# Performance work log

Hardware: AMD Instinct MI355X
Metric: run time of the kernel (lower is better)

## Reference

```python
import jax, jax.numpy as jnp
import numpy as np

INPUT_SIZE = 16
HIDDEN = 256


def setup_inputs() -> dict:
    key = jax.random.key(0)
    ks = jax.random.split(key, 12)
    B, T, F, H = 512, 168, INPUT_SIZE, HIDDEN
    s_ih = 1.0 / np.sqrt(H)
    def u(k, shape):
        return jax.random.uniform(k, shape, jnp.float32, -s_ih, s_ih)
    return {
        "x": jax.random.normal(ks[0], (B, T, F), jnp.float32),
        # LSTM params, torch gate order (i, f, g, o) stacked along dim 0
        "w_ih": u(ks[1], (4 * H, F)),
        "w_hh": u(ks[2], (4 * H, H)),
        "b_ih": u(ks[3], (4 * H,)),
        "b_hh": u(ks[4], (4 * H,)),
        # MLP params
        "fc1_w": u(ks[5], (128, H)),
        "fc1_b": u(ks[6], (128,)),
        "fc2_w": u(ks[7], (64, 128)),
        "fc2_b": u(ks[8], (64,)),
        "fc3_w": u(ks[9], (1, 64)),
        "fc3_b": u(ks[10], (1,)),
    }


def _lstm(x, w_ih, w_hh, b_ih, b_hh):
    B, T, F = x.shape
    H = w_hh.shape[1]
    # Precompute input contribution for all timesteps: [B, T, 4H]
    x_proj = jnp.einsum("btf,gf->btg", x, w_ih) + b_ih + b_hh

    def step(carry, xp_t):
        h, c = carry
        gates = xp_t + h @ w_hh.T  # [B, 4H]
        i, f, g, o = jnp.split(gates, 4, axis=-1)
        i = jax.nn.sigmoid(i)
        f = jax.nn.sigmoid(f)
        g = jnp.tanh(g)
        o = jax.nn.sigmoid(o)
        c = f * c + i * g
        h = o * jnp.tanh(c)
        return (h, c), h

    h0 = jnp.zeros((B, H), x.dtype)
    c0 = jnp.zeros((B, H), x.dtype)
    (_, _), hs = jax.lax.scan(step, (h0, c0), jnp.swapaxes(x_proj, 0, 1))
    return jnp.swapaxes(hs, 0, 1)  # [B, T, H]


def reference(x, w_ih, w_hh, b_ih, b_hh, fc1_w, fc1_b, fc2_w, fc2_b, fc3_w, fc3_b):
    h = _lstm(x, w_ih, w_hh, b_ih, b_hh)          # [B, T, H]
    h = jax.nn.relu(h @ fc1_w.T + fc1_b)           # [B, T, 128]
    h = jax.nn.relu(h @ fc2_w.T + fc2_b)           # [B, T, 64]
    out = h @ fc3_w.T + fc3_b                      # [B, T, 1]
    return out
```

## Files before the change

### kernel.cpp

```cpp
#include <hip/hip_runtime.h>

typedef _Float16 half8 __attribute__((ext_vector_type(8)));
typedef float floatx4 __attribute__((ext_vector_type(4)));
typedef unsigned uint4v __attribute__((ext_vector_type(4)));

#define Bsz 512
#define Tsz 168
#define Fsz 16
#define Hsz 256
#define KTILES 9
#define LDS_K 296

#define WSW_OFF   0
#define BIAS_OFF  589824
#define HH_OFF    675840
#define XBUF_OFF  (HH_OFF + 44040192)

__global__ __launch_bounds__(256) void k_prep(
    const float* __restrict__ w_hh, const float* __restrict__ w_ih,
    const float* __restrict__ b_ih, const float* __restrict__ b_hh,
    _Float16* __restrict__ wsw, float* __restrict__ bias) {
    const int b = blockIdx.x, tid = threadIdx.x;
    const int lane = tid & 63, sub = tid >> 6;
    if (b < 144) {
        int tile = b * 4 + sub;
        int nt = tile / KTILES, kt = tile - nt * KTILES;
        int n_in = lane & 15, kg = lane >> 4;
        int J = nt >> 2, g = nt & 3;
        int n_orig = g * 256 + J * 16 + n_in;
        half8 v;
#pragma unroll
        for (int e = 0; e < 8; ++e) {
            int k = kt * 32 + kg * 8 + e;
            float f;
            if (k < 256)      f = w_hh[n_orig * 256 + k];
            else if (k < 272) f = w_ih[n_orig * 16 + (k - 256)];
            else              f = 0.0f;
            v[e] = (_Float16)f;
        }
        ((half8*)wsw)[tile * 64 + lane] = v;
    } else {
        int id = (b - 144) * 256 + tid;
        int nt = id >> 4, n = id & 15;
        int J = nt >> 2, g = nt & 3;
        int n_orig = g * 256 + J * 16 + n;
        bias[id] = b_ih[n_orig] + b_hh[n_orig];
    }
}

__global__ __launch_bounds__(512, 2) void k_lstm16(
    const float* __restrict__ x, const _Float16* __restrict__ wsw,
    const float* __restrict__ bias, unsigned* __restrict__ hh32,
    unsigned long long* __restrict__ xbuf) {
    __shared__ __align__(16) _Float16 h_lds[16][LDS_K];
    __shared__ float glds[4][16][68];

    const int tid = threadIdx.x;
    const int wave = tid >> 6, lane = tid & 63;
    const int n_in = lane & 15, quad = lane >> 4;
    const int bb = blockIdx.x & 31, ng = blockIdx.x >> 5;
    const int b0 = bb * 16;
    const int Jl = wave & 3;
    const int gp = wave >> 2;

    float bs[2];
    uint4v wf[2][KTILES];
#pragma unroll
    for (int gg = 0; gg < 2; ++gg) {
        const int nt = ng * 16 + Jl * 4 + gp * 2 + gg;
        bs[gg] = bias[nt * 16 + n_in];
#pragma unroll
        for (int kt = 0; kt < KTILES; ++kt)
            wf[gg][kt] = ((const uint4v*)wsw)[((size_t)nt * KTILES + kt) * 64 + lane];
    }
#pragma unroll
    for (int gg = 0; gg < 2; ++gg) {
        asm volatile("" : "+v"(bs[gg]));
#pragma unroll
        for (int kt = 0; kt < KTILES; ++kt)
            asm volatile("" : "+v"(wf[gg][kt]));
    }

    for (int i = tid; i < 16 * LDS_K; i += 512)
        ((_Float16*)h_lds)[i] = (_Float16)0.0f;
    __syncthreads();
    if (tid < 256) {
        int m = tid >> 4, f = tid & 15;
        h_lds[m][Hsz + f] = (_Float16)x[((b0 + m) * Tsz + 0) * Fsz + f];
    }
    __syncthreads();

    const int cm = tid >> 5, cj = tid & 31;
    float c_st[2] = {0.f, 0.f};

    for (int t = 0; t < Tsz; ++t) {
        float xr = 0.0f;
        if (t + 1 < Tsz && tid < 256)
            xr = x[((b0 + (tid >> 4)) * Tsz + (t + 1)) * Fsz + (tid & 15)];

        half8 afr[KTILES];
#pragma unroll
        for (int kt = 0; kt < KTILES; ++kt)
            afr[kt] = *(const half8*)&h_lds[n_in][kt * 32 + quad * 8];

        floatx4 acc[2] = {(floatx4){0.f,0.f,0.f,0.f}, (floatx4){0.f,0.f,0.f,0.f}};
#pragma unroll
        for (int gg = 0; gg < 2; ++gg) {
#pragma unroll
            for (int kt = 0; kt < KTILES; ++kt)
                acc[gg] = __builtin_amdgcn_mfma_f32_16x16x32_f16(
                    afr[kt], __builtin_bit_cast(half8, wf[gg][kt]), acc[gg], 0, 0, 0);
        }

#pragma unroll
        for (int gg = 0; gg < 2; ++gg)
#pragma unroll
            for (int r = 0; r < 4; ++r)
                glds[gp * 2 + gg][quad * 4 + r][Jl * 16 + n_in] = acc[gg][r] + bs[gg];
        __syncthreads();

        union { _Float16 f[2]; unsigned u; } pk;
#pragma unroll
        for (int e = 0; e < 2; ++e) {
            int jl = 2 * cj + e;
            float ig = glds[0][cm][jl];
            float fg = glds[1][cm][jl];
            float gg_ = glds[2][cm][jl];
            float og = glds[3][cm][jl];
            float si = 1.0f / (1.0f + __expf(-ig));
            float sf = 1.0f / (1.0f + __expf(-fg));
            float tg = 1.0f - 2.0f / (__expf(2.0f * gg_) + 1.0f);
            float so = 1.0f / (1.0f + __expf(-og));
            float c = sf * c_st[e] + si * tg;
            c_st[e] = c;
            float th = 1.0f - 2.0f / (__expf(2.0f * c) + 1.0f);
            pk.f[e] = (_Float16)(so * th);
        }

        const size_t rb = ((size_t)((bb * 2 + (t & 1)) * 16));
        if (t + 1 < Tsz) {
            unsigned long long pv = ((unsigned long long)pk.u << 32) | (unsigned)(t + 1);
            __hip_atomic_store(&xbuf[(rb + cm) * 128 + ng * 32 + cj], pv,
                               __ATOMIC_RELAXED, __HIP_MEMORY_SCOPE_AGENT);
        }
        *(unsigned*)&h_lds[cm][ng * 64 + 2 * cj] = pk.u;
        __builtin_nontemporal_store(
            pk.u, &hh32[((size_t)(b0 + cm) * Tsz + t) * 128 + ng * 32 + cj]);

        if (t + 1 < Tsz) {
            const unsigned want = (unsigned)(t + 1);
            unsigned long long* p1 = &xbuf[(rb + cm) * 128 + ((ng + 1) & 3) * 32 + cj];
            unsigned long long* p2 = &xbuf[(rb + cm) * 128 + ((ng + 2) & 3) * 32 + cj];
            unsigned long long* p3 = &xbuf[(rb + cm) * 128 + ((ng + 3) & 3) * 32 + cj];
            unsigned long long v1 = __hip_atomic_load(p1, __ATOMIC_RELAXED,
                                                      __HIP_MEMORY_SCOPE_AGENT);
            unsigned long long v2 = __hip_atomic_load(p2, __ATOMIC_RELAXED,
                                                      __HIP_MEMORY_SCOPE_AGENT);
            unsigned long long v3 = __hip_atomic_load(p3, __ATOMIC_RELAXED,
                                                      __HIP_MEMORY_SCOPE_AGENT);
            while ((unsigned)v1 != want || (unsigned)v2 != want || (unsigned)v3 != want) {
                v1 = __hip_atomic_load(p1, __ATOMIC_RELAXED, __HIP_MEMORY_SCOPE_AGENT);
                v2 = __hip_atomic_load(p2, __ATOMIC_RELAXED, __HIP_MEMORY_SCOPE_AGENT);
                v3 = __hip_atomic_load(p3, __ATOMIC_RELAXED, __HIP_MEMORY_SCOPE_AGENT);
            }
            *(unsigned*)&h_lds[cm][((ng + 1) & 3) * 64 + 2 * cj] = (unsigned)(v1 >> 32);
            *(unsigned*)&h_lds[cm][((ng + 2) & 3) * 64 + 2 * cj] = (unsigned)(v2 >> 32);
            *(unsigned*)&h_lds[cm][((ng + 3) & 3) * 64 + 2 * cj] = (unsigned)(v3 >> 32);
            if (tid < 256)
                h_lds[tid >> 4][Hsz + (tid & 15)] = (_Float16)xr;
            __syncthreads();
        }
    }
}

__global__ __launch_bounds__(512, 2) void k_mlp6(
    const _Float16* __restrict__ hh, const float* __restrict__ fc1_w,
    const float* __restrict__ fc2_w, const float* __restrict__ b1,
    const float* __restrict__ b2, const float* __restrict__ w3,
    const float* __restrict__ b3, float* __restrict__ out) {
    __shared__ __align__(16) _Float16 w1sh[64 * 512];
    __shared__ __align__(16) _Float16 w2sh[16 * 512];
    __shared__ _Float16 st1[8][16][136];
    __shared__ _Float16 st2[8][16][72];

    const int tid = threadIdx.x;
    const int wave = tid >> 6, lane = tid & 63;
    const int n_in = lane & 15, quad = lane >> 4;

    {
#pragma unroll
        for (int it = 0; it < 8; ++it) {
            int s = it * 512 + tid;
            int tile = s >> 6, ln = s & 63;
            int nt = tile >> 3, kt = tile & 7, ni = ln & 15, kg = ln >> 4;
            const float* src = &fc1_w[(nt * 16 + ni) * 256 + kt * 32 + kg * 8];
            half8 v;
#pragma unroll
            for (int e = 0; e < 8; ++e) v[e] = (_Float16)src[e];
            ((half8*)w1sh)[s] = v;
        }
#pragma unroll
        for (int it = 0; it < 2; ++it) {
            int s = it * 512 + tid;
            int tile = s >> 6, ln = s & 63;
            int nt = tile >> 2, kt = tile & 3, ni = ln & 15, kg = ln >> 4;
            const float* src = &fc2_w[(nt * 16 + ni) * 128 + kt * 32 + kg * 8];
            half8 v;
#pragma unroll
            for (int e = 0; e < 8; ++e) v[e] = (_Float16)src[e];
            ((half8*)w2sh)[s] = v;
        }
    }
    __syncthreads();

    uint4v bufA[8], bufB[8], bufC[8];
    const int ch0 = blockIdx.x, ch1 = blockIdx.x + 224, ch2 = blockIdx.x + 448;

#define MLP_LOAD(dst, ch)                                                      \
    {                                                                          \
        const int tok0_ = (ch) * 128 + wave * 16;                              \
        _Pragma("unroll")                                                      \
        for (int kt = 0; kt < 8; ++kt)                                         \
            dst[kt] = __builtin_nontemporal_load(                              \
                (const uint4v*)&hh[(size_t)(tok0_ + n_in) * 256 + kt * 32 +    \
                                   quad * 8]);                                 \
    }

    MLP_LOAD(bufA, ch0)
    MLP_LOAD(bufB, ch1)
    MLP_LOAD(bufC, ch2)

    auto compute = [&](const uint4v* raw, int chunk) {
        const int tok0 = chunk * 128 + wave * 16;
        half8 afr[8];
#pragma unroll
        for (int kt = 0; kt < 8; ++kt)
            afr[kt] = __builtin_bit_cast(half8, raw[kt]);

#pragma unroll
        for (int nt = 0; nt < 8; ++nt) {
            floatx4 a = (floatx4){0.f, 0.f, 0.f, 0.f};
#pragma unroll
            for (int kt = 0; kt < 8; ++kt) {
                half8 bfr = *(const half8*)&w1sh[(nt * 8 + kt) * 512 + lane * 8];
                a = __builtin_amdgcn_mfma_f32_16x16x32_f16(afr[kt], bfr, a, 0, 0, 0);
            }
            float bbv = b1[nt * 16 + n_in];
#pragma unroll
            for (int r = 0; r < 4; ++r) {
                float v = a[r] + bbv;
                st1[wave][quad * 4 + r][nt * 16 + n_in] = (_Float16)(v > 0.f ? v : 0.f);
            }
        }

        half8 a2[4];
#pragma unroll
        for (int kt = 0; kt < 4; ++kt)
            a2[kt] = *(const half8*)&st1[wave][n_in][kt * 32 + quad * 8];
#pragma unroll
        for (int nt = 0; nt < 4; ++nt) {
            floatx4 a = (floatx4){0.f, 0.f, 0.f, 0.f};
#pragma unroll
            for (int kt = 0; kt < 4; ++kt) {
                half8 bfr = *(const half8*)&w2sh[(nt * 4 + kt) * 512 + lane * 8];
                a = __builtin_amdgcn_mfma_f32_16x16x32_f16(a2[kt], bfr, a, 0, 0, 0);
            }
            float bbv = b2[nt * 16 + n_in];
#pragma unroll
            for (int r = 0; r < 4; ++r) {
                float v = a[r] + bbv;
                st2[wave][quad * 4 + r][nt * 16 + n_in] = (_Float16)(v > 0.f ? v : 0.f);
            }
        }

        float p = 0.0f;
#pragma unroll
        for (int e = 0; e < 16; ++e)
            p += (float)st2[wave][n_in][quad * 16 + e] * w3[quad * 16 + e];
        p += __shfl_down(p, 32);
        p += __shfl_down(p, 16);
        if (quad == 0) out[tok0 + n_in] = p + b3[0];
    };

    compute(bufA, ch0);
    compute(bufB, ch1);
    compute(bufC, ch2);
#undef MLP_LOAD
}

extern "C" void kernel_launch(void* const* d_in, const int* in_sizes, int n_in,
                              void* d_out, int out_size, void* d_ws, size_t ws_size,
                              hipStream_t stream) {
    const float* x     = (const float*)d_in[0];
    const float* w_ih  = (const float*)d_in[1];
    const float* w_hh  = (const float*)d_in[2];
    const float* b_ih  = (const float*)d_in[3];
    const float* b_hh  = (const float*)d_in[4];
    const float* fc1_w = (const float*)d_in[5];
    const float* fc1_b = (const float*)d_in[6];
    const float* fc2_w = (const float*)d_in[7];
    const float* fc2_b = (const float*)d_in[8];
    const float* fc3_w = (const float*)d_in[9];
    const float* fc3_b = (const float*)d_in[10];

    char* ws = (char*)d_ws;
    _Float16* wsw  = (_Float16*)(ws + WSW_OFF);
    float*    bias = (float*)(ws + BIAS_OFF);
    _Float16* hhist= (_Float16*)(ws + HH_OFF);
    unsigned long long* xbuf = (unsigned long long*)(ws + XBUF_OFF);

    k_prep<<<148, 256, 0, stream>>>(w_hh, w_ih, b_ih, b_hh, wsw, bias);
    k_lstm16<<<128, 512, 0, stream>>>(x, wsw, bias, (unsigned*)hhist, xbuf);
    k_mlp6<<<224, 512, 0, stream>>>(hhist, fc1_w, fc2_w, fc1_b, fc2_b,
                                    fc3_w, fc3_b, (float*)d_out);
}
```

Before: 489.1 us.

## Split LSTM hidden dimension across eight blocks per batch tile instead of four

The recurrent LSTM kernel now launches 256 blocks, so eight blocks share a 16-row batch tile and each owns 32 hidden units, halving per-wave MFMA work and register-resident weights. Each block now polls seven peer slots per step instead of three in the global exchange buffer, and the xbuf row stride doubles. This aims to shorten each sequential step's compute on the critical path by using more CUs, at the cost of more cross-block synchronisation traffic and polling latency. The x prefetch was also moved after the h store.

```diff
diff --git a/kernel.cpp b/kernel.cpp
--- a/kernel.cpp
+++ b/kernel.cpp
@@ -48,38 +48,27 @@
     }
 }
 
-__global__ __launch_bounds__(512, 2) void k_lstm16(
+__global__ __launch_bounds__(512, 1) void k_lstm17(
     const float* __restrict__ x, const _Float16* __restrict__ wsw,
     const float* __restrict__ bias, unsigned* __restrict__ hh32,
     unsigned long long* __restrict__ xbuf) {
     __shared__ __align__(16) _Float16 h_lds[16][LDS_K];
-    __shared__ float glds[4][16][68];
+    __shared__ float glds[4][16][36];
 
     const int tid = threadIdx.x;
     const int wave = tid >> 6, lane = tid & 63;
     const int n_in = lane & 15, quad = lane >> 4;
     const int bb = blockIdx.x & 31, ng = blockIdx.x >> 5;
     const int b0 = bb * 16;
-    const int Jl = wave & 3;
-    const int gp = wave >> 2;
-
-    float bs[2];
-    uint4v wf[2][KTILES];
-#pragma unroll
-    for (int gg = 0; gg < 2; ++gg) {
-        const int nt = ng * 16 + Jl * 4 + gp * 2 + gg;
-        bs[gg] = bias[nt * 16 + n_in];
-#pragma unroll
-        for (int kt = 0; kt < KTILES; ++kt)
-            wf[gg][kt] = ((const uint4v*)wsw)[((size_t)nt * KTILES + kt) * 64 + lane];
-    }
-#pragma unroll
-    for (int gg = 0; gg < 2; ++gg) {
-        asm volatile("" : "+v"(bs[gg]));
-#pragma unroll
-        for (int kt = 0; kt < KTILES; ++kt)
-            asm volatile("" : "+v"(wf[gg][kt]));
-    }
+    const int Jl = wave & 1;
+    const int g  = wave >> 1;
+    const int nt = (ng * 2 + Jl) * 4 + g;
+
+    const float bs = bias[nt * 16 + n_in];
+    half8 wf[KTILES];
+#pragma unroll
+    for (int kt = 0; kt < KTILES; ++kt)
+        wf[kt] = ((const half8*)wsw)[((size_t)nt * KTILES + kt) * 64 + lane];
 
     for (int i = tid; i < 16 * LDS_K; i += 512)
         ((_Float16*)h_lds)[i] = (_Float16)0.0f;
@@ -91,81 +80,81 @@
     __syncthreads();
 
     const int cm = tid >> 5, cj = tid & 31;
-    float c_st[2] = {0.f, 0.f};
+    float c_st = 0.f;
+    unsigned short* hh16 = (unsigned short*)hh32;
 
     for (int t = 0; t < Tsz; ++t) {
-        float xr = 0.0f;
-        if (t + 1 < Tsz && tid < 256)
-            xr = x[((b0 + (tid >> 4)) * Tsz + (t + 1)) * Fsz + (tid & 15)];
-
         half8 afr[KTILES];
 #pragma unroll
         for (int kt = 0; kt < KTILES; ++kt)
             afr[kt] = *(const half8*)&h_lds[n_in][kt * 32 + quad * 8];
 
-        floatx4 acc[2] = {(floatx4){0.f,0.f,0.f,0.f}, (floatx4){0.f,0.f,0.f,0.f}};
-#pragma unroll
-        for (int gg = 0; gg < 2; ++gg) {
-#pragma unroll
-            for (int kt = 0; kt < KTILES; ++kt)
-                acc[gg] = __builtin_amdgcn_mfma_f32_16x16x32_f16(
-                    afr[kt], __builtin_bit_cast(half8, wf[gg][kt]), acc[gg], 0, 0, 0);
-        }
-
-#pragma unroll
-        for (int gg = 0; gg < 2; ++gg)
-#pragma unroll
-            for (int r = 0; r < 4; ++r)
-                glds[gp * 2 + gg][quad * 4 + r][Jl * 16 + n_in] = acc[gg][r] + bs[gg];
+        floatx4 acc = (floatx4){0.f, 0.f, 0.f, 0.f};
+#pragma unroll
+        for (int kt = 0; kt < KTILES; ++kt)
+            acc = __builtin_amdgcn_mfma_f32_16x16x32_f16(afr[kt], wf[kt], acc, 0, 0, 0);
+
+#pragma unroll
+        for (int r = 0; r < 4; ++r)
+            glds[g][quad * 4 + r][Jl * 16 + n_in] = acc[r] + bs;
         __syncthreads();
 
-        union { _Float16 f[2]; unsigned u; } pk;
-#pragma unroll
-        for (int e = 0; e < 2; ++e) {
-            int jl = 2 * cj + e;
-            float ig = glds[0][cm][jl];
-            float fg = glds[1][cm][jl];
-            float gg_ = glds[2][cm][jl];
-            float og = glds[3][cm][jl];
-            float si = 1.0f / (1.0f + __expf(-ig));
-            float sf = 1.0f / (1.0f + __expf(-fg));
-            float tg = 1.0f - 2.0f / (__expf(2.0f * gg_) + 1.0f);
-            float so = 1.0f / (1.0f + __expf(-og));
-            float c = sf * c_st[e] + si * tg;
-            c_st[e] = c;
-            float th = 1.0f - 2.0f / (__expf(2.0f * c) + 1.0f);
-            pk.f[e] = (_Float16)(so * th);
-        }
+        float ig = glds[0][cm][cj];
+        float fg = glds[1][cm][cj];
+        float gv = glds[2][cm][cj];
+        float og = glds[3][cm][cj];
+        float si = 1.0f / (1.0f + __expf(-ig));
+        float sf = 1.0f / (1.0f + __expf(-fg));
+        float tg = 1.0f - 2.0f / (__expf(2.0f * gv) + 1.0f);
+        float so = 1.0f / (1.0f + __expf(-og));
+        float c = sf * c_st + si * tg;
+        c_st = c;
+        float th = 1.0f - 2.0f / (__expf(2.0f * c) + 1.0f);
+        _Float16 hval = (_Float16)(so * th);
+        unsigned short hu = __builtin_bit_cast(unsigned short, hval);
+
+        h_lds[cm][ng * 32 + cj] = hval;
 
         const size_t rb = ((size_t)((bb * 2 + (t & 1)) * 16));
         if (t + 1 < Tsz) {
-            unsigned long long pv = ((unsigned long long)pk.u << 32) | (unsigned)(t + 1);
-            __hip_atomic_store(&xbuf[(rb + cm) * 128 + ng * 32 + cj], pv,
+            unsigned long long pv =
+                ((unsigned long long)hu << 32) | (unsigned)(t + 1);
+            __hip_atomic_store(&xbuf[(rb + cm) * 256 + ng * 32 + cj], pv,
                                __ATOMIC_RELAXED, __HIP_MEMORY_SCOPE_AGENT);
         }
-        *(unsigned*)&h_lds[cm][ng * 64 + 2 * cj] = pk.u;
         __builtin_nontemporal_store(
-            pk.u, &hh32[((size_t)(b0 + cm) * Tsz + t) * 128 + ng * 32 + cj]);
+            hu, &hh16[((size_t)(b0 + cm) * Tsz + t) * 256 + ng * 32 + cj]);
 
         if (t + 1 < Tsz) {
+            float xr = 0.0f;
+            if (tid < 256)
+                xr = x[((b0 + (tid >> 4)) * Tsz + (t + 1)) * Fsz + (tid & 15)];
+
             const unsigned want = (unsigned)(t + 1);
-            unsigned long long* p1 = &xbuf[(rb + cm) * 128 + ((ng + 1) & 3) * 32 + cj];
-            unsigned long long* p2 = &xbuf[(rb + cm) * 128 + ((ng + 2) & 3) * 32 + cj];
-            unsigned long long* p3 = &xbuf[(rb + cm) * 128 + ((ng + 3) & 3) * 32 + cj];
-            unsigned long long v1 = __hip_atomic_load(p1, __ATOMIC_RELAXED,
-                                                      __HIP_MEMORY_SCOPE_AGENT);
-            unsigned long long v2 = __hip_atomic_load(p2, __ATOMIC_RELAXED,
-                                                      __HIP_MEMORY_SCOPE_AGENT);
-            unsigned long long v3 = __hip_atomic_load(p3, __ATOMIC_RELAXED,
-                                                      __HIP_MEMORY_SCOPE_AGENT);
-            while ((unsigned)v1 != want || (unsigned)v2 != want || (unsigned)v3 != want) {
-                v1 = __hip_atomic_load(p1, __ATOMIC_RELAXED, __HIP_MEMORY_SCOPE_AGENT);
-                v2 = __hip_atomic_load(p2, __ATOMIC_RELAXED, __HIP_MEMORY_SCOPE_AGENT);
-                v3 = __hip_atomic_load(p3, __ATOMIC_RELAXED, __HIP_MEMORY_SCOPE_AGENT);
-            }
-            *(unsigned*)&h_lds[cm][((ng + 1) & 3) * 64 + 2 * cj] = (unsigned)(v1 >> 32);
-            *(unsigned*)&h_lds[cm][((ng + 2) & 3) * 64 + 2 * cj] = (unsigned)(v2 >> 32);
-            *(unsigned*)&h_lds[cm][((ng + 3) & 3) * 64 + 2 * cj] = (unsigned)(v3 >> 32);
+            unsigned long long* pp[7];
+            unsigned long long vv[7];
+#pragma unroll
+            for (int k = 0; k < 7; ++k)
+                pp[k] = &xbuf[(rb + cm) * 256 + ((ng + k + 1) & 7) * 32 + cj];
+#pragma unroll
+            for (int k = 0; k < 7; ++k)
+                vv[k] = __hip_atomic_load(pp[k], __ATOMIC_RELAXED,
+                                          __HIP_MEMORY_SCOPE_AGENT);
+            while (true) {
+                bool ok = true;
+#pragma unroll
+                for (int k = 0; k < 7; ++k) ok &= ((unsigned)vv[k] == want);
+                if (ok) break;
+#pragma unroll
+                for (int k = 0; k < 7; ++k)
+                    if ((unsigned)vv[k] != want)
+                        vv[k] = __hip_atomic_load(pp[k], __ATOMIC_RELAXED,
+                                                  __HIP_MEMORY_SCOPE_AGENT);
+            }
+#pragma unroll
+            for (int k = 0; k < 7; ++k)
+                h_lds[cm][((ng + k + 1) & 7) * 32 + cj] = __builtin_bit_cast(
+                    _Float16, (unsigned short)(vv[k] >> 32));
             if (tid < 256)
                 h_lds[tid >> 4][Hsz + (tid & 15)] = (_Float16)xr;
             __syncthreads();
@@ -310,7 +299,7 @@
     unsigned long long* xbuf = (unsigned long long*)(ws + XBUF_OFF);
 
     k_prep<<<148, 256, 0, stream>>>(w_hh, w_ih, b_ih, b_hh, wsw, bias);
-    k_lstm16<<<128, 512, 0, stream>>>(x, wsw, bias, (unsigned*)hhist, xbuf);
+    k_lstm17<<<256, 512, 0, stream>>>(x, wsw, bias, (unsigned*)hhist, xbuf);
     k_mlp6<<<224, 512, 0, stream>>>(hhist, fc1_w, fc2_w, fc1_b, fc2_b,
                                     fc3_w, fc3_b, (float*)d_out);
 }
```

Measured after the change: 458.6 us. 1.07x faster.

## Process two batch tiles per LSTM block, halving grid and sharing weight registers

Applied to the files above, without the earlier changes.

Each LSTM block now handles two 16-row batch tiles (A and B) with the same register-resident W_hh slice, so the grid shrinks from 128 to 64 blocks and each weight fragment is reused twice. The point is to cut the number of cross-block spin-sync participants and to let tile B's compute overlap with tile A's exchange latency. In exchange, each block does twice the serial work per timestep, launch bounds drop to one block per CU, and the asm register pinning of the weights is removed.

```diff
diff --git a/kernel.cpp b/kernel.cpp
--- a/kernel.cpp
+++ b/kernel.cpp
@@ -48,126 +48,194 @@
     }
 }
 
-__global__ __launch_bounds__(512, 2) void k_lstm16(
+__global__ __launch_bounds__(512, 1) void k_lstm18(
     const float* __restrict__ x, const _Float16* __restrict__ wsw,
     const float* __restrict__ bias, unsigned* __restrict__ hh32,
     unsigned long long* __restrict__ xbuf) {
-    __shared__ __align__(16) _Float16 h_lds[16][LDS_K];
-    __shared__ float glds[4][16][68];
+    __shared__ __align__(16) _Float16 hA[16][LDS_K];
+    __shared__ __align__(16) _Float16 hB[16][LDS_K];
+    __shared__ float gA[4][16][68];
+    __shared__ float gB[4][16][68];
 
     const int tid = threadIdx.x;
     const int wave = tid >> 6, lane = tid & 63;
     const int n_in = lane & 15, quad = lane >> 4;
-    const int bb = blockIdx.x & 31, ng = blockIdx.x >> 5;
-    const int b0 = bb * 16;
+    const int p = blockIdx.x & 15, ng = blockIdx.x >> 4;
+    const int bbA = 2 * p, bbB = 2 * p + 1;
+    const int b0A = bbA * 16, b0B = bbB * 16;
     const int Jl = wave & 3;
     const int gp = wave >> 2;
 
     float bs[2];
-    uint4v wf[2][KTILES];
+    half8 wf[2][KTILES];
 #pragma unroll
     for (int gg = 0; gg < 2; ++gg) {
         const int nt = ng * 16 + Jl * 4 + gp * 2 + gg;
         bs[gg] = bias[nt * 16 + n_in];
 #pragma unroll
         for (int kt = 0; kt < KTILES; ++kt)
-            wf[gg][kt] = ((const uint4v*)wsw)[((size_t)nt * KTILES + kt) * 64 + lane];
-    }
-#pragma unroll
-    for (int gg = 0; gg < 2; ++gg) {
-        asm volatile("" : "+v"(bs[gg]));
-#pragma unroll
-        for (int kt = 0; kt < KTILES; ++kt)
-            asm volatile("" : "+v"(wf[gg][kt]));
-    }
-
-    for (int i = tid; i < 16 * LDS_K; i += 512)
-        ((_Float16*)h_lds)[i] = (_Float16)0.0f;
+            wf[gg][kt] = ((const half8*)wsw)[((size_t)nt * KTILES + kt) * 64 + lane];
+    }
+
+    for (int i = tid; i < 16 * LDS_K; i += 512) {
+        ((_Float16*)hA)[i] = (_Float16)0.0f;
+        ((_Float16*)hB)[i] = (_Float16)0.0f;
+    }
     __syncthreads();
-    if (tid < 256) {
-        int m = tid >> 4, f = tid & 15;
-        h_lds[m][Hsz + f] = (_Float16)x[((b0 + m) * Tsz + 0) * Fsz + f];
+    {
+        int m = (tid & 255) >> 4, f = tid & 15;
+        if (tid < 256) hA[m][Hsz + f] = (_Float16)x[((b0A + m) * Tsz + 0) * Fsz + f];
+        else           hB[m][Hsz + f] = (_Float16)x[((b0B + m) * Tsz + 0) * Fsz + f];
     }
     __syncthreads();
 
     const int cm = tid >> 5, cj = tid & 31;
-    float c_st[2] = {0.f, 0.f};
+    float cA[2] = {0.f, 0.f}, cB[2] = {0.f, 0.f};
 
     for (int t = 0; t < Tsz; ++t) {
         float xr = 0.0f;
-        if (t + 1 < Tsz && tid < 256)
-            xr = x[((b0 + (tid >> 4)) * Tsz + (t + 1)) * Fsz + (tid & 15)];
-
-        half8 afr[KTILES];
-#pragma unroll
-        for (int kt = 0; kt < KTILES; ++kt)
-            afr[kt] = *(const half8*)&h_lds[n_in][kt * 32 + quad * 8];
-
-        floatx4 acc[2] = {(floatx4){0.f,0.f,0.f,0.f}, (floatx4){0.f,0.f,0.f,0.f}};
-#pragma unroll
-        for (int gg = 0; gg < 2; ++gg) {
+        if (t + 1 < Tsz) {
+            int m = (tid & 255) >> 4, f = tid & 15;
+            xr = (tid < 256)
+                ? x[((b0A + m) * Tsz + (t + 1)) * Fsz + f]
+                : x[((b0B + m) * Tsz + (t + 1)) * Fsz + f];
+        }
+
+        {
+            half8 afr[KTILES];
 #pragma unroll
             for (int kt = 0; kt < KTILES; ++kt)
-                acc[gg] = __builtin_amdgcn_mfma_f32_16x16x32_f16(
-                    afr[kt], __builtin_bit_cast(half8, wf[gg][kt]), acc[gg], 0, 0, 0);
-        }
-
-#pragma unroll
-        for (int gg = 0; gg < 2; ++gg)
-#pragma unroll
-            for (int r = 0; r < 4; ++r)
-                glds[gp * 2 + gg][quad * 4 + r][Jl * 16 + n_in] = acc[gg][r] + bs[gg];
+                afr[kt] = *(const half8*)&hA[n_in][kt * 32 + quad * 8];
+            floatx4 acc[2] = {(floatx4){0.f,0.f,0.f,0.f}, (floatx4){0.f,0.f,0.f,0.f}};
+#pragma unroll
+            for (int gg = 0; gg < 2; ++gg)
+#pragma unroll
+                for (int kt = 0; kt < KTILES; ++kt)
+                    acc[gg] = __builtin_amdgcn_mfma_f32_16x16x32_f16(
+                        afr[kt], wf[gg][kt], acc[gg], 0, 0, 0);
+#pragma unroll
+            for (int gg = 0; gg < 2; ++gg)
+#pragma unroll
+                for (int r = 0; r < 4; ++r)
+                    gA[gp * 2 + gg][quad * 4 + r][Jl * 16 + n_in] = acc[gg][r] + bs[gg];
+        }
         __syncthreads();
 
-        union { _Float16 f[2]; unsigned u; } pk;
-#pragma unroll
-        for (int e = 0; e < 2; ++e) {
-            int jl = 2 * cj + e;
-            float ig = glds[0][cm][jl];
-            float fg = glds[1][cm][jl];
-            float gg_ = glds[2][cm][jl];
-            float og = glds[3][cm][jl];
-            float si = 1.0f / (1.0f + __expf(-ig));
-            float sf = 1.0f / (1.0f + __expf(-fg));
-            float tg = 1.0f - 2.0f / (__expf(2.0f * gg_) + 1.0f);
-            float so = 1.0f / (1.0f + __expf(-og));
-            float c = sf * c_st[e] + si * tg;
-            c_st[e] = c;
-            float th = 1.0f - 2.0f / (__expf(2.0f * c) + 1.0f);
-            pk.f[e] = (_Float16)(so * th);
-        }
-
-        const size_t rb = ((size_t)((bb * 2 + (t & 1)) * 16));
-        if (t + 1 < Tsz) {
-            unsigned long long pv = ((unsigned long long)pk.u << 32) | (unsigned)(t + 1);
-            __hip_atomic_store(&xbuf[(rb + cm) * 128 + ng * 32 + cj], pv,
-                               __ATOMIC_RELAXED, __HIP_MEMORY_SCOPE_AGENT);
-        }
-        *(unsigned*)&h_lds[cm][ng * 64 + 2 * cj] = pk.u;
-        __builtin_nontemporal_store(
-            pk.u, &hh32[((size_t)(b0 + cm) * Tsz + t) * 128 + ng * 32 + cj]);
+        {
+            union { _Float16 f[2]; unsigned u; } pk;
+#pragma unroll
+            for (int e = 0; e < 2; ++e) {
+                int jl = 2 * cj + e;
+                float ig = gA[0][cm][jl], fg = gA[1][cm][jl];
+                float gv = gA[2][cm][jl], og = gA[3][cm][jl];
+                float si = 1.0f / (1.0f + __expf(-ig));
+                float sf = 1.0f / (1.0f + __expf(-fg));
+                float tg = 1.0f - 2.0f / (__expf(2.0f * gv) + 1.0f);
+                float so = 1.0f / (1.0f + __expf(-og));
+                float c = sf * cA[e] + si * tg;
+                cA[e] = c;
+                float th = 1.0f - 2.0f / (__expf(2.0f * c) + 1.0f);
+                pk.f[e] = (_Float16)(so * th);
+            }
+            const size_t rbA = (size_t)((bbA * 2 + (t & 1)) * 16);
+            if (t + 1 < Tsz) {
+                unsigned long long pv = ((unsigned long long)pk.u << 32) | (unsigned)(t + 1);
+                __hip_atomic_store(&xbuf[(rbA + cm) * 128 + ng * 32 + cj], pv,
+                                   __ATOMIC_RELAXED, __HIP_MEMORY_SCOPE_AGENT);
+            }
+            *(unsigned*)&hA[cm][ng * 64 + 2 * cj] = pk.u;
+            __builtin_nontemporal_store(
+                pk.u, &hh32[((size_t)(b0A + cm) * Tsz + t) * 128 + ng * 32 + cj]);
+        }
+
+        {
+            half8 afr[KTILES];
+#pragma unroll
+            for (int kt = 0; kt < KTILES; ++kt)
+                afr[kt] = *(const half8*)&hB[n_in][kt * 32 + quad * 8];
+            floatx4 acc[2] = {(floatx4){0.f,0.f,0.f,0.f}, (floatx4){0.f,0.f,0.f,0.f}};
+#pragma unroll
+            for (int gg = 0; gg < 2; ++gg)
+#pragma unroll
+                for (int kt = 0; kt < KTILES; ++kt)
+                    acc[gg] = __builtin_amdgcn_mfma_f32_16x16x32_f16(
+                        afr[kt], wf[gg][kt], acc[gg], 0, 0, 0);
+#pragma unroll
+            for (int gg = 0; gg < 2; ++gg)
+#pragma unroll
+                for (int r = 0; r < 4; ++r)
+                    gB[gp * 2 + gg][quad * 4 + r][Jl * 16 + n_in] = acc[gg][r] + bs[gg];
+        }
+        __syncthreads();
+
+        {
+            union { _Float16 f[2]; unsigned u; } pk;
+#pragma unroll
+            for (int e = 0; e < 2; ++e) {
+                int jl = 2 * cj + e;
+                float ig = gB[0][cm][jl], fg = gB[1][cm][jl];
+                float gv = gB[2][cm][jl], og = gB[3][cm][jl];
+                float si = 1.0f / (1.0f + __expf(-ig));
+                float sf = 1.0f / (1.0f + __expf(-fg));
+                float tg = 1.0f - 2.0f / (__expf(2.0f * gv) + 1.0f);
+                float so = 1.0f / (1.0f + __expf(-og));
+                float c = sf * cB[e] + si * tg;
+                cB[e] = c;
+                float th = 1.0f - 2.0f / (__expf(2.0f * c) + 1.0f);
+                pk.f[e] = (_Float16)(so * th);
+            }
+            const size_t rbB = (size_t)((bbB * 2 + (t & 1)) * 16);
+            if (t + 1 < Tsz) {
+                unsigned long long pv = ((unsigned long long)pk.u << 32) | (unsigned)(t + 1);
+                __hip_atomic_store(&xbuf[(rbB + cm) * 128 + ng * 32 + cj], pv,
+                                   __ATOMIC_RELAXED, __HIP_MEMORY_SCOPE_AGENT);
+            }
+            *(unsigned*)&hB[cm][ng * 64 + 2 * cj] = pk.u;
+            __builtin_nontemporal_store(
+                pk.u, &hh32[((size_t)(b0B + cm) * Tsz + t) * 128 + ng * 32 + cj]);
+        }
 
         if (t + 1 < Tsz) {
             const unsigned want = (unsigned)(t + 1);
-            unsigned long long* p1 = &xbuf[(rb + cm) * 128 + ((ng + 1) & 3) * 32 + cj];
-            unsigned long long* p2 = &xbuf[(rb + cm) * 128 + ((ng + 2) & 3) * 32 + cj];
-            unsigned long long* p3 = &xbuf[(rb + cm) * 128 + ((ng + 3) & 3) * 32 + cj];
-            unsigned long long v1 = __hip_atomic_load(p1, __ATOMIC_RELAXED,
-                                                      __HIP_MEMORY_SCOPE_AGENT);
-            unsigned long long v2 = __hip_atomic_load(p2, __ATOMIC_RELAXED,
-                                                      __HIP_MEMORY_SCOPE_AGENT);
-            unsigned long long v3 = __hip_atomic_load(p3, __ATOMIC_RELAXED,
-                                                      __HIP_MEMORY_SCOPE_AGENT);
-            while ((unsigned)v1 != want || (unsigned)v2 != want || (unsigned)v3 != want) {
-                v1 = __hip_atomic_load(p1, __ATOMIC_RELAXED, __HIP_MEMORY_SCOPE_AGENT);
-                v2 = __hip_atomic_load(p2, __ATOMIC_RELAXED, __HIP_MEMORY_SCOPE_AGENT);
-                v3 = __hip_atomic_load(p3, __ATOMIC_RELAXED, __HIP_MEMORY_SCOPE_AGENT);
-            }
-            *(unsigned*)&h_lds[cm][((ng + 1) & 3) * 64 + 2 * cj] = (unsigned)(v1 >> 32);
-            *(unsigned*)&h_lds[cm][((ng + 2) & 3) * 64 + 2 * cj] = (unsigned)(v2 >> 32);
-            *(unsigned*)&h_lds[cm][((ng + 3) & 3) * 64 + 2 * cj] = (unsigned)(v3 >> 32);
-            if (tid < 256)
-                h_lds[tid >> 4][Hsz + (tid & 15)] = (_Float16)xr;
+            {
+                const size_t rbA = (size_t)((bbA * 2 + (t & 1)) * 16);
+                unsigned long long* p1 = &xbuf[(rbA + cm) * 128 + ((ng + 1) & 3) * 32 + cj];
+                unsigned long long* p2 = &xbuf[(rbA + cm) * 128 + ((ng + 2) & 3) * 32 + cj];
+                unsigned long long* p3 = &xbuf[(rbA + cm) * 128 + ((ng + 3) & 3) * 32 + cj];
+                unsigned long long v1 = __hip_atomic_load(p1, __ATOMIC_RELAXED, __HIP_MEMORY_SCOPE_AGENT);
+                unsigned long long v2 = __hip_atomic_load(p2, __ATOMIC_RELAXED, __HIP_MEMORY_SCOPE_AGENT);
+                unsigned long long v3 = __hip_atomic_load(p3, __ATOMIC_RELAXED, __HIP_MEMORY_SCOPE_AGENT);
+                while ((unsigned)v1 != want || (unsigned)v2 != want || (unsigned)v3 != want) {
+                    v1 = __hip_atomic_load(p1, __ATOMIC_RELAXED, __HIP_MEMORY_SCOPE_AGENT);
+                    v2 = __hip_atomic_load(p2, __ATOMIC_RELAXED, __HIP_MEMORY_SCOPE_AGENT);
+                    v3 = __hip_atomic_load(p3, __ATOMIC_RELAXED, __HIP_MEMORY_SCOPE_AGENT);
+                }
+                *(unsigned*)&hA[cm][((ng + 1) & 3) * 64 + 2 * cj] = (unsigned)(v1 >> 32);
+                *(unsigned*)&hA[cm][((ng + 2) & 3) * 64 + 2 * cj] = (unsigned)(v2 >> 32);
+                *(unsigned*)&hA[cm][((ng + 3) & 3) * 64 + 2 * cj] = (unsigned)(v3 >> 32);
+            }
+            {
+                const size_t rbB = (size_t)((bbB * 2 + (t & 1)) * 16);
+                unsigned long long* p1 = &xbuf[(rbB + cm) * 128 + ((ng + 1) & 3) * 32 + cj];
+                unsigned long long* p2 = &xbuf[(rbB + cm) * 128 + ((ng + 2) & 3) * 32 + cj];
+                unsigned long long* p3 = &xbuf[(rbB + cm) * 128 + ((ng + 3) & 3) * 32 + cj];
+                unsigned long long v1 = __hip_atomic_load(p1, __ATOMIC_RELAXED, __HIP_MEMORY_SCOPE_AGENT);
+                unsigned long long v2 = __hip_atomic_load(p2, __ATOMIC_RELAXED, __HIP_MEMORY_SCOPE_AGENT);
+                unsigned long long v3 = __hip_atomic_load(p3, __ATOMIC_RELAXED, __HIP_MEMORY_SCOPE_AGENT);
+                while ((unsigned)v1 != want || (unsigned)v2 != want || (unsigned)v3 != want) {
+                    v1 = __hip_atomic_load(p1, __ATOMIC_RELAXED, __HIP_MEMORY_SCOPE_AGENT);
+                    v2 = __hip_atomic_load(p2, __ATOMIC_RELAXED, __HIP_MEMORY_SCOPE_AGENT);
+                    v3 = __hip_atomic_load(p3, __ATOMIC_RELAXED, __HIP_MEMORY_SCOPE_AGENT);
+                }
+                *(unsigned*)&hB[cm][((ng + 1) & 3) * 64 + 2 * cj] = (unsigned)(v1 >> 32);
+                *(unsigned*)&hB[cm][((ng + 2) & 3) * 64 + 2 * cj] = (unsigned)(v2 >> 32);
+                *(unsigned*)&hB[cm][((ng + 3) & 3) * 64 + 2 * cj] = (unsigned)(v3 >> 32);
+            }
+            {
+                int m = (tid & 255) >> 4, f = tid & 15;
+                if (tid < 256) hA[m][Hsz + f] = (_Float16)xr;
+                else           hB[m][Hsz + f] = (_Float16)xr;
+            }
             __syncthreads();
         }
     }
@@ -310,7 +378,7 @@
     unsigned long long* xbuf = (unsigned long long*)(ws + XBUF_OFF);
 
     k_prep<<<148, 256, 0, stream>>>(w_hh, w_ih, b_ih, b_hh, wsw, bias);
-    k_lstm16<<<128, 512, 0, stream>>>(x, wsw, bias, (unsigned*)hhist, xbuf);
+    k_lstm18<<<64, 512, 0, stream>>>(x, wsw, bias, (unsigned*)hhist, xbuf);
     k_mlp6<<<224, 512, 0, stream>>>(hhist, fc1_w, fc2_w, fc1_b, fc2_b,
                                     fc3_w, fc3_b, (float*)d_out);
 }
```

Result: slower. 657.2 us (+34.4%).

## Reload LSTM weights from cache each step via inline asm instead of holding registers

Applied to the files above, without the earlier changes.

The recurrent weight fragments are no longer kept resident in VGPRs across all timesteps. They are re-issued as global_load_dwordx4 instructions in inline asm after each step's output store, overlapping with the cross-block spin-wait. Launch bounds drop to one block per CU, the x prefetch moves after the store, and the spin loop re-polls only flags not yet ready. The aim is to cut register pressure and spills, at the cost of extra L2 traffic every step and reliance on asm results being ready before the next MFMA.

```diff
diff --git a/kernel.cpp b/kernel.cpp
--- a/kernel.cpp
+++ b/kernel.cpp
@@ -48,7 +48,34 @@
     }
 }
 
-__global__ __launch_bounds__(512, 2) void k_lstm16(
+#define WPREFETCH()                                                            \
+    asm volatile(                                                              \
+        "global_load_dwordx4 %0, %18, off\n\t"                                 \
+        "global_load_dwordx4 %1, %18, off offset:1024\n\t"                     \
+        "global_load_dwordx4 %2, %18, off offset:2048\n\t"                     \
+        "global_load_dwordx4 %3, %18, off offset:3072\n\t"                     \
+        "global_load_dwordx4 %4, %19, off\n\t"                                 \
+        "global_load_dwordx4 %5, %19, off offset:1024\n\t"                     \
+        "global_load_dwordx4 %6, %19, off offset:2048\n\t"                     \
+        "global_load_dwordx4 %7, %19, off offset:3072\n\t"                     \
+        "global_load_dwordx4 %8, %20, off\n\t"                                 \
+        "global_load_dwordx4 %9, %21, off\n\t"                                 \
+        "global_load_dwordx4 %10, %21, off offset:1024\n\t"                    \
+        "global_load_dwordx4 %11, %21, off offset:2048\n\t"                    \
+        "global_load_dwordx4 %12, %21, off offset:3072\n\t"                    \
+        "global_load_dwordx4 %13, %22, off\n\t"                                \
+        "global_load_dwordx4 %14, %22, off offset:1024\n\t"                    \
+        "global_load_dwordx4 %15, %22, off offset:2048\n\t"                    \
+        "global_load_dwordx4 %16, %22, off offset:3072\n\t"                    \
+        "global_load_dwordx4 %17, %23, off\n\t"                                \
+        : "=&v"(wf[0][0]), "=&v"(wf[0][1]), "=&v"(wf[0][2]), "=&v"(wf[0][3]),  \
+          "=&v"(wf[0][4]), "=&v"(wf[0][5]), "=&v"(wf[0][6]), "=&v"(wf[0][7]),  \
+          "=&v"(wf[0][8]), "=&v"(wf[1][0]), "=&v"(wf[1][1]), "=&v"(wf[1][2]),  \
+          "=&v"(wf[1][3]), "=&v"(wf[1][4]), "=&v"(wf[1][5]), "=&v"(wf[1][6]),  \
+          "=&v"(wf[1][7]), "=&v"(wf[1][8])                                     \
+        : "v"(a00), "v"(a01), "v"(a02), "v"(a10), "v"(a11), "v"(a12))
+
+__global__ __launch_bounds__(512, 1) void k_lstm19(
     const float* __restrict__ x, const _Float16* __restrict__ wsw,
     const float* __restrict__ bias, unsigned* __restrict__ hh32,
     unsigned long long* __restrict__ xbuf) {
@@ -63,23 +90,21 @@
     const int Jl = wave & 3;
     const int gp = wave >> 2;
 
+    const int nt0 = ng * 16 + Jl * 4 + gp * 2 + 0;
+    const int nt1 = ng * 16 + Jl * 4 + gp * 2 + 1;
+    const char* wb = (const char*)wsw;
+    unsigned long long a00 = (unsigned long long)(wb + nt0 * 9216 + lane * 16);
+    unsigned long long a01 = a00 + 4096;
+    unsigned long long a02 = a00 + 8192;
+    unsigned long long a10 = (unsigned long long)(wb + nt1 * 9216 + lane * 16);
+    unsigned long long a11 = a10 + 4096;
+    unsigned long long a12 = a10 + 8192;
     float bs[2];
+    bs[0] = bias[nt0 * 16 + n_in];
+    bs[1] = bias[nt1 * 16 + n_in];
+
     uint4v wf[2][KTILES];
-#pragma unroll
-    for (int gg = 0; gg < 2; ++gg) {
-        const int nt = ng * 16 + Jl * 4 + gp * 2 + gg;
-        bs[gg] = bias[nt * 16 + n_in];
-#pragma unroll
-        for (int kt = 0; kt < KTILES; ++kt)
-            wf[gg][kt] = ((const uint4v*)wsw)[((size_t)nt * KTILES + kt) * 64 + lane];
-    }
-#pragma unroll
-    for (int gg = 0; gg < 2; ++gg) {
-        asm volatile("" : "+v"(bs[gg]));
-#pragma unroll
-        for (int kt = 0; kt < KTILES; ++kt)
-            asm volatile("" : "+v"(wf[gg][kt]));
-    }
+    WPREFETCH();
 
     for (int i = tid; i < 16 * LDS_K; i += 512)
         ((_Float16*)h_lds)[i] = (_Float16)0.0f;
@@ -94,10 +119,6 @@
     float c_st[2] = {0.f, 0.f};
 
     for (int t = 0; t < Tsz; ++t) {
-        float xr = 0.0f;
-        if (t + 1 < Tsz && tid < 256)
-            xr = x[((b0 + (tid >> 4)) * Tsz + (t + 1)) * Fsz + (tid & 15)];
-
         half8 afr[KTILES];
 #pragma unroll
         for (int kt = 0; kt < KTILES; ++kt)
@@ -136,6 +157,7 @@
             float th = 1.0f - 2.0f / (__expf(2.0f * c) + 1.0f);
             pk.f[e] = (_Float16)(so * th);
         }
+        *(unsigned*)&h_lds[cm][ng * 64 + 2 * cj] = pk.u;
 
         const size_t rb = ((size_t)((bb * 2 + (t & 1)) * 16));
         if (t + 1 < Tsz) {
@@ -143,11 +165,16 @@
             __hip_atomic_store(&xbuf[(rb + cm) * 128 + ng * 32 + cj], pv,
                                __ATOMIC_RELAXED, __HIP_MEMORY_SCOPE_AGENT);
         }
-        *(unsigned*)&h_lds[cm][ng * 64 + 2 * cj] = pk.u;
         __builtin_nontemporal_store(
             pk.u, &hh32[((size_t)(b0 + cm) * Tsz + t) * 128 + ng * 32 + cj]);
 
         if (t + 1 < Tsz) {
+            WPREFETCH();
+
+            float xr = 0.0f;
+            if (tid < 256)
+                xr = x[((b0 + (tid >> 4)) * Tsz + (t + 1)) * Fsz + (tid & 15)];
+
             const unsigned want = (unsigned)(t + 1);
             unsigned long long* p1 = &xbuf[(rb + cm) * 128 + ((ng + 1) & 3) * 32 + cj];
             unsigned long long* p2 = &xbuf[(rb + cm) * 128 + ((ng + 2) & 3) * 32 + cj];
@@ -159,9 +186,12 @@
             unsigned long long v3 = __hip_atomic_load(p3, __ATOMIC_RELAXED,
                                                       __HIP_MEMORY_SCOPE_AGENT);
             while ((unsigned)v1 != want || (unsigned)v2 != want || (unsigned)v3 != want) {
-                v1 = __hip_atomic_load(p1, __ATOMIC_RELAXED, __HIP_MEMORY_SCOPE_AGENT);
-                v2 = __hip_atomic_load(p2, __ATOMIC_RELAXED, __HIP_MEMORY_SCOPE_AGENT);
-                v3 = __hip_atomic_load(p3, __ATOMIC_RELAXED, __HIP_MEMORY_SCOPE_AGENT);
+                if ((unsigned)v1 != want)
+                    v1 = __hip_atomic_load(p1, __ATOMIC_RELAXED, __HIP_MEMORY_SCOPE_AGENT);
+                if ((unsigned)v2 != want)
+                    v2 = __hip_atomic_load(p2, __ATOMIC_RELAXED, __HIP_MEMORY_SCOPE_AGENT);
+                if ((unsigned)v3 != want)
+                    v3 = __hip_atomic_load(p3, __ATOMIC_RELAXED, __HIP_MEMORY_SCOPE_AGENT);
             }
             *(unsigned*)&h_lds[cm][((ng + 1) & 3) * 64 + 2 * cj] = (unsigned)(v1 >> 32);
             *(unsigned*)&h_lds[cm][((ng + 2) & 3) * 64 + 2 * cj] = (unsigned)(v2 >> 32);
@@ -310,7 +340,7 @@
     unsigned long long* xbuf = (unsigned long long*)(ws + XBUF_OFF);
 
     k_prep<<<148, 256, 0, stream>>>(w_hh, w_ih, b_ih, b_hh, wsw, bias);
-    k_lstm16<<<128, 512, 0, stream>>>(x, wsw, bias, (unsigned*)hhist, xbuf);
+    k_lstm19<<<128, 512, 0, stream>>>(x, wsw, bias, (unsigned*)hhist, xbuf);
     k_mlp6<<<224, 512, 0, stream>>>(hhist, fc1_w, fc2_w, fc1_b, fc2_b,
                                     fc3_w, fc3_b, (float*)d_out);
 }
```

After: 558.7 us. 1.14x slower.
